# Performance work log

Measured on AMD Instinct MI355X. Metric: run time of the kernel, lower is better.

## Reference

```python
import jax, jax.numpy as jnp
import numpy as np

K_EFF = 8           # top-k factors selected per token (init k, < num_factors)
TEMPERATURE = 1.0   # forward() default


def setup_inputs() -> dict:
    key = jax.random.key(0)
    k1, k2 = jax.random.split(key)
    N, M = 131072, 512
    logits = jax.random.normal(k1, (N, M), dtype=jnp.float32)
    beta_qb = jax.random.normal(k2, (M,), dtype=jnp.float32)
    return {"logits": logits, "beta_qb": beta_qb}


def reference(logits, beta_qb):
    """Quantile-balanced sparse gating forward (eval path).

    Top-k selection on debiased logits (logits - beta_qb); probabilities are a
    softmax over the selected RAW logits, scattered back to a dense [N, M] map.
    """
    N, M = logits.shape
    # debiased scores only steer the hard top-k selection
    scores_adj = logits - beta_qb[None, :]                 # [N, M]
    _, topk_idx = jax.lax.top_k(scores_adj, K_EFF)         # [N, k]
    # gather raw logits at selected factors, softmax over the k slots
    selected = jnp.take_along_axis(logits, topk_idx, axis=-1)   # [N, k]
    selected_probs = jax.nn.softmax(selected / TEMPERATURE, axis=-1)
    # scatter sparse probabilities back into dense [N, M]
    rows = jnp.arange(N)[:, None]                          # [N, 1]
    probs = jnp.zeros_like(logits).at[rows, topk_idx].set(selected_probs)
    return probs
```

## Files before the change

### kernel.cpp

```cpp
#include <hip/hip_runtime.h>


constexpr int M_DIM = 512;
constexpr int KSEL  = 8;

__global__ __launch_bounds__(256, 8)
void qb_gating_kernel(const float* __restrict__ logits,
                      const float* __restrict__ beta,
                      float* __restrict__ out,
                      int nrows)
{
    const int lane  = threadIdx.x & 63;
    const int gwave = (int)((blockIdx.x * blockDim.x + threadIdx.x) >> 6);
    const int nwaves = (int)((gridDim.x * blockDim.x) >> 6);

    const int base0 = 4 * lane;
    const int base1 = 256 + 4 * lane;

    const float4 b0 = *(const float4*)(beta + base0);
    const float4 b1 = *(const float4*)(beta + base1);

    int gidx[8];
#pragma unroll
    for (int s = 0; s < 8; ++s)
        gidx[s] = (s < 4) ? (base0 + s) : (base1 + (s - 4));

    for (int row = gwave; row < nrows; row += nwaves) {
        const float* rp = logits + (size_t)row * M_DIM;
        const float4 r0 = *(const float4*)(rp + base0);
        const float4 r1 = *(const float4*)(rp + base1);

        float raw[8] = {r0.x, r0.y, r0.z, r0.w, r1.x, r1.y, r1.z, r1.w};
        float adj[8] = {r0.x - b0.x, r0.y - b0.y, r0.z - b0.z, r0.w - b0.w,
                        r1.x - b1.x, r1.y - b1.y, r1.z - b1.z, r1.w - b1.w};

        int   sel_g[KSEL];
        float sel_raw[KSEL];

#pragma unroll
        for (int t = 0; t < KSEL; ++t) {
            float lv = adj[0]; float lr = raw[0]; int lg = gidx[0];
#pragma unroll
            for (int s = 1; s < 8; ++s) {
                bool better = adj[s] > lv;
                lv = better ? adj[s] : lv;
                lr = better ? raw[s] : lr;
                lg = better ? gidx[s] : lg;
            }
            float v = lv; int g = lg;
#pragma unroll
            for (int off = 32; off > 0; off >>= 1) {
                float ov = __shfl_xor(v, off, 64);
                int   og = __shfl_xor(g, off, 64);
                bool take = (ov > v) || (ov == v && og < g);
                v = take ? ov : v;
                g = take ? og : g;
            }
            int olane = (g & 255) >> 2;
            float rv = __shfl(lr, olane, 64);
            sel_g[t]   = g;
            sel_raw[t] = rv;
#pragma unroll
            for (int s = 0; s < 8; ++s)
                if (gidx[s] == g) adj[s] = -__builtin_inff();
        }

        float m = sel_raw[0];
#pragma unroll
        for (int t = 1; t < KSEL; ++t) m = fmaxf(m, sel_raw[t]);
        float e[KSEL]; float sum = 0.f;
#pragma unroll
        for (int t = 0; t < KSEL; ++t) { e[t] = __expf(sel_raw[t] - m); sum += e[t]; }
        const float inv = 1.0f / sum;

        float o[8] = {0.f,0.f,0.f,0.f,0.f,0.f,0.f,0.f};
#pragma unroll
        for (int t = 0; t < KSEL; ++t) {
            const float p = e[t] * inv;
            const int   g = sel_g[t];
#pragma unroll
            for (int s = 0; s < 8; ++s)
                o[s] = (gidx[s] == g) ? p : o[s];
        }

        float* op = out + (size_t)row * M_DIM;
        *(float4*)(op + base0) = make_float4(o[0], o[1], o[2], o[3]);
        *(float4*)(op + base1) = make_float4(o[4], o[5], o[6], o[7]);
    }
}

extern "C" void kernel_launch(void* const* d_in, const int* in_sizes, int n_in,
                              void* d_out, int out_size, void* d_ws, size_t ws_size,
                              hipStream_t stream)
{
    const float* logits = (const float*)d_in[0];
    const float* beta   = (const float*)d_in[1];
    float*       out    = (float*)d_out;

    const int nrows = in_sizes[0] / M_DIM;

    qb_gating_kernel<<<4096, 256, 0, stream>>>(logits, beta, out, nrows);
}
```

Baseline: 492.5 us.

## Replace per-round shuffle argmax with per-slot DPP max and ballot selection

Turns the debiased scores into order-preserving unsigned keys and keeps one wave-wide maximum per register slot, computed with DPP row operations and readlane. Each top-k round then picks the best slot, finds the winning lane with a ballot, and re-reduces only that slot, instead of doing a full 6-step two-value shuffle butterfly per round. Selected entries are marked by zeroing their key, so the output is built by recomputing exp on the raw values. It also swaps the division for a reciprocal intrinsic. Ties now resolve by lowest lane within a slot rather than lowest global index, and any element whose key is exactly 0 would be treated as selected.

After: 449.9 us. -8.7%, faster.

```diff
diff --git a/kernel.cpp b/kernel.cpp
--- a/kernel.cpp
+++ b/kernel.cpp
@@ -2,7 +2,34 @@
 
 
 constexpr int M_DIM = 512;
-constexpr int KSEL  = 8;
+
+template<int CTRL, int RMASK>
+__device__ __forceinline__ unsigned wmax_step(unsigned v) {
+    int y = __builtin_amdgcn_update_dpp((int)v, (int)v, CTRL, RMASK, 0xF, false);
+    unsigned u = (unsigned)y;
+    return u > v ? u : v;
+}
+
+__device__ __forceinline__ unsigned wave_max_u32(unsigned v) {
+    v = wmax_step<0x111, 0xF>(v);
+    v = wmax_step<0x112, 0xF>(v);
+    v = wmax_step<0x114, 0xF>(v);
+    v = wmax_step<0x118, 0xF>(v);
+    v = wmax_step<0x142, 0xA>(v);
+    v = wmax_step<0x143, 0xC>(v);
+    return (unsigned)__builtin_amdgcn_readlane((int)v, 63);
+}
+
+template<int S>
+__device__ __forceinline__ void round_step(unsigned key[8], const float raw[8],
+                                           unsigned M[8], unsigned win,
+                                           float& rawt, int lane, bool rereduce) {
+    unsigned long long mm = __ballot(key[S] == win);
+    int wl = (int)__builtin_ctzll(mm);
+    rawt = __int_as_float(__builtin_amdgcn_readlane(__float_as_int(raw[S]), wl));
+    if (lane == wl) key[S] = 0u;
+    if (rereduce) M[S] = wave_max_u32(key[S]);
+}
 
 __global__ __launch_bounds__(256, 8)
 void qb_gating_kernel(const float* __restrict__ logits,
@@ -10,8 +37,8 @@
                       float* __restrict__ out,
                       int nrows)
 {
-    const int lane  = threadIdx.x & 63;
-    const int gwave = (int)((blockIdx.x * blockDim.x + threadIdx.x) >> 6);
+    const int lane   = threadIdx.x & 63;
+    const int gwave  = (int)((blockIdx.x * blockDim.x + threadIdx.x) >> 6);
     const int nwaves = (int)((gridDim.x * blockDim.x) >> 6);
 
     const int base0 = 4 * lane;
@@ -19,69 +46,54 @@
 
     const float4 b0 = *(const float4*)(beta + base0);
     const float4 b1 = *(const float4*)(beta + base1);
-
-    int gidx[8];
-#pragma unroll
-    for (int s = 0; s < 8; ++s)
-        gidx[s] = (s < 4) ? (base0 + s) : (base1 + (s - 4));
+    const float bb[8] = {b0.x, b0.y, b0.z, b0.w, b1.x, b1.y, b1.z, b1.w};
 
     for (int row = gwave; row < nrows; row += nwaves) {
         const float* rp = logits + (size_t)row * M_DIM;
         const float4 r0 = *(const float4*)(rp + base0);
         const float4 r1 = *(const float4*)(rp + base1);
+        float raw[8] = {r0.x, r0.y, r0.z, r0.w, r1.x, r1.y, r1.z, r1.w};
 
-        float raw[8] = {r0.x, r0.y, r0.z, r0.w, r1.x, r1.y, r1.z, r1.w};
-        float adj[8] = {r0.x - b0.x, r0.y - b0.y, r0.z - b0.z, r0.w - b0.w,
-                        r1.x - b1.x, r1.y - b1.y, r1.z - b1.z, r1.w - b1.w};
+        unsigned key[8];
+#pragma unroll
+        for (int s = 0; s < 8; ++s) {
+            const float a = raw[s] - bb[s];
+            const int u = __float_as_int(a);
+            key[s] = (unsigned)(u ^ ((u >> 31) | 0x80000000));
+        }
 
-        int   sel_g[KSEL];
-        float sel_raw[KSEL];
+        unsigned M[8];
+#pragma unroll
+        for (int s = 0; s < 8; ++s) M[s] = wave_max_u32(key[s]);
 
+        float sraw[8];
 #pragma unroll
-        for (int t = 0; t < KSEL; ++t) {
-            float lv = adj[0]; float lr = raw[0]; int lg = gidx[0];
+        for (int t = 0; t < 8; ++t) {
+            unsigned best = M[0]; int ss = 0;
 #pragma unroll
             for (int s = 1; s < 8; ++s) {
-                bool better = adj[s] > lv;
-                lv = better ? adj[s] : lv;
-                lr = better ? raw[s] : lr;
-                lg = better ? gidx[s] : lg;
+                if (M[s] > best) { best = M[s]; ss = s; }
             }
-            float v = lv; int g = lg;
-#pragma unroll
-            for (int off = 32; off > 0; off >>= 1) {
-                float ov = __shfl_xor(v, off, 64);
-                int   og = __shfl_xor(g, off, 64);
-                bool take = (ov > v) || (ov == v && og < g);
-                v = take ? ov : v;
-                g = take ? og : g;
+#define ROUND_CASE(S) case S: round_step<S>(key, raw, M, best, sraw[t], lane, t < 7); break;
+            switch (ss) {
+                ROUND_CASE(0) ROUND_CASE(1) ROUND_CASE(2) ROUND_CASE(3)
+                ROUND_CASE(4) ROUND_CASE(5) ROUND_CASE(6) ROUND_CASE(7)
             }
-            int olane = (g & 255) >> 2;
-            float rv = __shfl(lr, olane, 64);
-            sel_g[t]   = g;
-            sel_raw[t] = rv;
-#pragma unroll
-            for (int s = 0; s < 8; ++s)
-                if (gidx[s] == g) adj[s] = -__builtin_inff();
+#undef ROUND_CASE
         }
 
-        float m = sel_raw[0];
+        float m = sraw[0];
 #pragma unroll
-        for (int t = 1; t < KSEL; ++t) m = fmaxf(m, sel_raw[t]);
-        float e[KSEL]; float sum = 0.f;
+        for (int t = 1; t < 8; ++t) m = fmaxf(m, sraw[t]);
+        float sum = 0.f;
 #pragma unroll
-        for (int t = 0; t < KSEL; ++t) { e[t] = __expf(sel_raw[t] - m); sum += e[t]; }
-        const float inv = 1.0f / sum;
+        for (int t = 0; t < 8; ++t) sum += __expf(sraw[t] - m);
+        const float inv = __builtin_amdgcn_rcpf(sum);
 
-        float o[8] = {0.f,0.f,0.f,0.f,0.f,0.f,0.f,0.f};
+        float o[8];
 #pragma unroll
-        for (int t = 0; t < KSEL; ++t) {
-            const float p = e[t] * inv;
-            const int   g = sel_g[t];
-#pragma unroll
-            for (int s = 0; s < 8; ++s)
-                o[s] = (gidx[s] == g) ? p : o[s];
-        }
+        for (int s = 0; s < 8; ++s)
+            o[s] = (key[s] == 0u) ? __expf(raw[s] - m) * inv : 0.f;
 
         float* op = out + (size_t)row * M_DIM;
         *(float4*)(op + base0) = make_float4(o[0], o[1], o[2], o[3]);
```
